# Performance work log

Measured on AMD Instinct MI355X. Metric: run time of the kernel, lower is better.

Reference implementation:

```python
import jax, jax.numpy as jnp
import numpy as np

B, R, H, IN, L = 8, 128, 256, 512, 3
NH, DH = 4, H // 4  # attention heads


def _layernorm(x, g, b, eps=1e-5):
    mu = jnp.mean(x, axis=-1, keepdims=True)
    var = jnp.mean(jnp.square(x - mu), axis=-1, keepdims=True)
    return (x - mu) * jax.lax.rsqrt(var + eps) * g + b


def setup_inputs() -> dict:
    key = jax.random.key(0)
    ks = iter(jax.random.split(key, 40))
    s = 0.02
    d = {}
    d['x'] = jax.random.normal(next(ks), (B, IN), jnp.float32)
    d['We'] = jax.random.normal(next(ks), (IN, H), jnp.float32) * s
    d['be'] = jnp.zeros((H,), jnp.float32)
    # per-graph-layer params, stacked along leading L axis
    d['msg_W1'] = jax.random.normal(next(ks), (L, 2 * H, H), jnp.float32) * s
    d['msg_b1'] = jnp.zeros((L, H), jnp.float32)
    d['msg_W2'] = jax.random.normal(next(ks), (L, H, H), jnp.float32) * s
    d['msg_b2'] = jnp.zeros((L, H), jnp.float32)
    d['upd_W1'] = jax.random.normal(next(ks), (L, 2 * H, H), jnp.float32) * s
    d['upd_b1'] = jnp.zeros((L, H), jnp.float32)
    d['upd_W2'] = jax.random.normal(next(ks), (L, H, H), jnp.float32) * s
    d['upd_b2'] = jnp.zeros((L, H), jnp.float32)
    d['ln_g'] = jnp.ones((L, H), jnp.float32)
    d['ln_b'] = jnp.zeros((L, H), jnp.float32)
    d['rule_adj'] = jax.random.normal(next(ks), (R, R), jnp.float32)
    # multihead attention (4 heads)
    d['Wq'] = jax.random.normal(next(ks), (H, H), jnp.float32) * s
    d['bq'] = jnp.zeros((H,), jnp.float32)
    d['Wk'] = jax.random.normal(next(ks), (H, H), jnp.float32) * s
    d['bk'] = jnp.zeros((H,), jnp.float32)
    d['Wv'] = jax.random.normal(next(ks), (H, H), jnp.float32) * s
    d['bv'] = jnp.zeros((H,), jnp.float32)
    d['Wo'] = jax.random.normal(next(ks), (H, H), jnp.float32) * s
    d['bo'] = jnp.zeros((H,), jnp.float32)
    # readout MLP -> num_rules logits
    d['ro_W1'] = jax.random.normal(next(ks), (H, H), jnp.float32) * s
    d['ro_b1'] = jnp.zeros((H,), jnp.float32)
    d['ro_W2'] = jax.random.normal(next(ks), (H, R), jnp.float32) * s
    d['ro_b2'] = jnp.zeros((R,), jnp.float32)
    return d


def reference(x, We, be, msg_W1, msg_b1, msg_W2, msg_b2,
              upd_W1, upd_b1, upd_W2, upd_b2, ln_g, ln_b, rule_adj,
              Wq, bq, Wk, bk, Wv, bv, Wo, bo,
              ro_W1, ro_b1, ro_W2, ro_b2):
    # node encoder, broadcast to all rule-graph nodes: [B,R,H]
    h0 = x @ We + be
    h = jnp.broadcast_to(h0[:, None, :], (B, R, H))
    # rule adjacency with self-edges excluded (loop used i != j)
    A = jax.nn.sigmoid(rule_adj) * (1.0 - jnp.eye(R, dtype=rule_adj.dtype))  # [R,R]
    for l in range(L):
        # message_net(cat(h_i, h_j)) = relu(h_i@W1a + h_j@W1b + b1)@W2 + b2
        W1a, W1b = msg_W1[l][:H], msg_W1[l][H:]
        a = h @ W1a   # [B,R,H] (receiver i part)
        bb = h @ W1b  # [B,R,H] (sender j part)
        pre = jax.nn.relu(a[:, :, None, :] + bb[:, None, :, :] + msg_b1[l])  # [B,R,R,H]
        m = pre @ msg_W2[l] + msg_b2[l]  # [B,R,R,H] message from j to i
        agg = jnp.einsum('bijh,ij->bih', m, A)  # weighted sum over senders j
        # update_net(cat(h, agg))
        Wu1a, Wu1b = upd_W1[l][:H], upd_W1[l][H:]
        u = jax.nn.relu(h @ Wu1a + agg @ Wu1b + upd_b1[l]) @ upd_W2[l] + upd_b2[l]
        h = _layernorm(h + u, ln_g[l], ln_b[l])
    # multihead self-attention over nodes
    q = (h @ Wq + bq).reshape(B, R, NH, DH)
    k = (h @ Wk + bk).reshape(B, R, NH, DH)
    v = (h @ Wv + bv).reshape(B, R, NH, DH)
    logits = jnp.einsum('bqhd,bkhd->bhqk', q, k) / jnp.sqrt(jnp.float32(DH))
    attn = jax.nn.softmax(logits, axis=-1)
    pooled = jnp.einsum('bhqk,bkhd->bqhd', attn, v).reshape(B, R, H) @ Wo + bo
    g = jnp.mean(pooled, axis=1)  # [B,H]
    rule_logits = jax.nn.relu(g @ ro_W1 + ro_b1) @ ro_W2 + ro_b2
    rule_probabilities = jax.nn.softmax(rule_logits, axis=-1)  # [B,R]
    return rule_probabilities
```

## Files before the change

### kernel.cpp

```cpp
#include <hip/hip_runtime.h>
#include <math.h>

constexpr int NB  = 8;
constexpr int NR  = 128;
constexpr int HID = 256;
constexpr int NIN = 512;
constexpr int DHD = 64;
constexpr size_t SZ = (size_t)NB * NR * HID;

struct KP {
    const float *x, *We, *be, *msg_W1, *msg_b1, *msg_W2, *msg_b2;
    const float *upd_W1, *upd_b1, *upd_W2, *upd_b2, *ln_g, *ln_b, *rule_adj;
    const float *Wq, *bq, *Wk, *bk, *Wv, *bv, *Wo, *bo, *ro_W1, *ro_b1, *ro_W2, *ro_b2;
    float* out;
    float *N0, *N1, *N2;
    float *aB, *bbB, *p1B;
    float *aA, *bbA, *p1A;
    float *W2u, *mb2u, *Aw, *rsum;
    float *mW1s;
    float *h0g;
    float *gacc;
    float *scratch;
};

__device__ __forceinline__ void gemm_core(
    float (&As)[16][68], float (&Bs)[16][64], int m0, int n0,
    const float* __restrict__ A, const float* __restrict__ B,
    float (&acc)[4][4])
{
    int tid = threadIdx.x;
    int ty = tid >> 4, tx = tid & 15;
    int arow = tid >> 2, acol = (tid & 3) << 2;
    int brow = tid >> 4, bcol = (tid & 15) << 2;
    int m = m0 + arow;

    float4 av = *(const float4*)&A[(size_t)m * HID + acol];
    float4 bv = *(const float4*)&B[(size_t)brow * HID + n0 + bcol];

    for (int k0 = 0; k0 < HID; k0 += 16) {
        As[acol + 0][arow] = av.x;
        As[acol + 1][arow] = av.y;
        As[acol + 2][arow] = av.z;
        As[acol + 3][arow] = av.w;
        *(float4*)&Bs[brow][bcol] = bv;
        __syncthreads();
        if (k0 + 16 < HID) {
            av = *(const float4*)&A[(size_t)m * HID + k0 + 16 + acol];
            bv = *(const float4*)&B[(size_t)(k0 + 16 + brow) * HID + n0 + bcol];
        }
#pragma unroll
        for (int kk = 0; kk < 16; ++kk) {
            float4 af = *(const float4*)&As[kk][ty << 2];
            float4 bf = *(const float4*)&Bs[kk][tx << 2];
            float a_[4] = {af.x, af.y, af.z, af.w};
            float b_[4] = {bf.x, bf.y, bf.z, bf.w};
#pragma unroll
            for (int i = 0; i < 4; ++i)
#pragma unroll
                for (int j = 0; j < 4; ++j) acc[i][j] += a_[i] * b_[j];
        }
        __syncthreads();
    }
}

__device__ __forceinline__ void gemv256w(
    const float* xs, const float* __restrict__ W,
    const float* __restrict__ bias, int relu, float* ys, float* red)
{
    int tid = threadIdx.x;
    int w = tid >> 6, l = tid & 63;
    float4 acc = {0.f, 0.f, 0.f, 0.f};
    const float* Wp = W + (size_t)(w * 64) * HID + l * 4;
    const float* xp = xs + w * 64;
#pragma unroll 16
    for (int kk = 0; kk < 64; ++kk) {
        float xv = xp[kk];
        float4 wv = *(const float4*)(Wp + (size_t)kk * HID);
        acc.x += xv * wv.x; acc.y += xv * wv.y;
        acc.z += xv * wv.z; acc.w += xv * wv.w;
    }
    *(float4*)&red[w * 256 + l * 4] = acc;
    __syncthreads();
    float v = red[tid] + red[256 + tid] + red[512 + tid] + red[768 + tid];
    if (bias) v += bias[tid];
    if (relu) v = fmaxf(v, 0.0f);
    ys[tid] = v;
    __syncthreads();
}

__device__ __forceinline__ void rows4_q(
    const float (&rows)[4][HID], const float* __restrict__ W,
    int col, int q, float o[4])
{
    o[0] = o[1] = o[2] = o[3] = 0.f;
    int kb = q * 64;
#pragma unroll 4
    for (int k0 = 0; k0 < 64; k0 += 4) {
        int k = kb + k0;
        float w0 = W[(size_t)(k + 0) * HID + col];
        float w1 = W[(size_t)(k + 1) * HID + col];
        float w2 = W[(size_t)(k + 2) * HID + col];
        float w3 = W[(size_t)(k + 3) * HID + col];
#pragma unroll
        for (int ii = 0; ii < 4; ++ii) {
            float4 rv = *(const float4*)&rows[ii][k];
            o[ii] += rv.x * w0 + rv.y * w1 + rv.z * w2 + rv.w * w3;
        }
    }
}

__device__ __forceinline__ float gemv_q(
    const float* xs, const float* __restrict__ W, int col, int q)
{
    float o = 0.f;
    int kb = q * 64;
#pragma unroll 8
    for (int k = 0; k < 64; ++k)
        o += xs[kb + k] * W[(size_t)(kb + k) * HID + col];
    return o;
}

__device__ __forceinline__ void ln_stats4_q(
    float (&sred)[4][4][2], float (&mi)[4][2], const float v[4], int q)
{
    if (q == 0) {
        int w = threadIdx.x >> 6, l = threadIdx.x & 63;
        float s[4], qq[4];
#pragma unroll
        for (int ii = 0; ii < 4; ++ii) { s[ii] = v[ii]; qq[ii] = v[ii] * v[ii]; }
#pragma unroll
        for (int off = 32; off; off >>= 1) {
#pragma unroll
            for (int ii = 0; ii < 4; ++ii) {
                s[ii] += __shfl_xor(s[ii], off);
                qq[ii] += __shfl_xor(qq[ii], off);
            }
        }
        if (l == 0) {
#pragma unroll
            for (int ii = 0; ii < 4; ++ii) { sred[w][ii][0] = s[ii]; sred[w][ii][1] = qq[ii]; }
        }
    }
    __syncthreads();
    if (threadIdx.x < 4) {
        int r = threadIdx.x;
        float ss = sred[0][r][0] + sred[1][r][0] + sred[2][r][0] + sred[3][r][0];
        float qq = sred[0][r][1] + sred[1][r][1] + sred[2][r][1] + sred[3][r][1];
        float mu = ss * (1.0f / HID);
        mi[r][0] = mu;
        mi[r][1] = rsqrtf(qq * (1.0f / HID) - mu * mu + 1e-5f);
    }
    __syncthreads();
}

__global__ __launch_bounds__(256) void setup0_kernel(KP P) {
    __shared__ union {
        struct { float As[16][68]; float Bs[16][64]; } g;
        struct { float xs[NIN]; float part[8][32]; } e;
    } L;
    int blk = blockIdx.x;
    int t = threadIdx.x;

    if (blk < 32) {
        int rr = blk * 4 + (t >> 6);
        int l = t & 63;
        float s_loc = 0.f;
#pragma unroll
        for (int rep = 0; rep < 2; ++rep) {
            int j = l + rep * 64;
            float xv = P.rule_adj[rr * NR + j];
            float sg = 1.0f / (1.0f + expf(-xv));
            if (j == rr) sg = 0.0f;
            P.Aw[rr * NR + j] = sg;
            s_loc += sg;
        }
#pragma unroll
        for (int off = 32; off; off >>= 1) s_loc += __shfl_xor(s_loc, off);
        if (l == 0) P.rsum[rr] = s_loc;
    } else if (blk < 80) {
        int idx = blk - 32, l2 = idx >> 4, t16 = idx & 15;
        int m0 = (t16 >> 2) * 64, n0 = (t16 & 3) * 64;
        float acc[4][4] = {};
        gemm_core(L.g.As, L.g.Bs, m0, n0,
                  P.msg_W2 + (size_t)l2 * HID * HID,
                  P.upd_W1 + (size_t)l2 * 2 * HID * HID + (size_t)HID * HID,
                  acc);
        int ty = t >> 4, tx = t & 15;
        float* C = P.W2u + (size_t)l2 * HID * HID;
#pragma unroll
        for (int i = 0; i < 4; ++i) {
            int m = m0 + (ty << 2) + i, n = n0 + (tx << 2);
            float4 o = {acc[i][0], acc[i][1], acc[i][2], acc[i][3]};
            *(float4*)&C[(size_t)m * HID + n] = o;
        }
    } else if (blk < 83) {
        int l2 = blk - 80;
        const float* b2v = P.msg_b2 + l2 * HID;
        const float* Bm = P.upd_W1 + (size_t)l2 * 2 * HID * HID + (size_t)HID * HID;
        float acc = 0.f;
#pragma unroll 4
        for (int k = 0; k < HID; ++k) acc += b2v[k] * Bm[(size_t)k * HID + t];
        P.mb2u[l2 * HID + t] = acc;
    } else if (blk < 147) {
        int idx = blk - 83;
        int b = idx >> 3, s = idx & 7;
        L.e.xs[t]       = P.x[b * NIN + t];
        L.e.xs[256 + t] = P.x[b * NIN + 256 + t];
        __syncthreads();
        int c = t & 31, seg = t >> 5;
        int col = s * 32 + c;
        const float* Wp = P.We + (size_t)(seg * 64) * HID + col;
        const float* xp = L.e.xs + seg * 64;
        float acc = 0.f;
#pragma unroll 16
        for (int k = 0; k < 64; ++k) acc += xp[k] * Wp[(size_t)k * HID];
        L.e.part[seg][c] = acc;
        __syncthreads();
        if (t < 32) {
            float v = 0.f;
#pragma unroll
            for (int sg = 0; sg < 8; ++sg) v += L.e.part[sg][t];
            int cc = s * 32 + t;
            P.h0g[b * HID + cc] = v + P.be[cc];
        }
    } else if (blk < 163) {
        int base = (blk - 147) * 4096;
        for (int i = t; i < 4096; i += 256) {
            int o = base + i;
            P.mW1s[o] = P.msg_W1[o] + P.msg_W1[65536 + o];
        }
    } else {
        int pfid = blk - 163, npf = 256 - 163;
        const float* arr[11] = {P.We, P.msg_W1, P.msg_W2, P.upd_W1, P.upd_W2,
                                P.Wq, P.Wk, P.Wv, P.Wo, P.ro_W1, P.ro_W2};
        const int n4[11] = {32768, 98304, 49152, 98304, 49152,
                            16384, 16384, 16384, 16384, 16384, 8192};
        float s = 0.f;
        for (int a = 0; a < 11; ++a) {
            const float4* p4 = (const float4*)arr[a];
            for (int i = pfid * 256 + t; i < n4[a]; i += npf * 256) {
                float4 v = p4[i];
                s += v.x + v.y + v.z + v.w;
            }
        }
        if (s == 1.0e37f) P.scratch[pfid] = s;
    }
}

__global__ __launch_bounds__(1024) void layer0p_kernel(KP P) {
    __shared__ float h0s[HID], p0s[HID], c0s[HID], c1s[HID];
    __shared__ float u1s[4][HID];
    __shared__ float nrm[4][HID];
    __shared__ float part4[4][4][HID];
    __shared__ float sred[4][4][2];
    __shared__ float mi[4][2];
    int blk = blockIdx.x;
    int m0 = blk * 4;
    int b = m0 >> 7, i0 = m0 & 127;
    int t = threadIdx.x;
    int col = t & 255, q = t >> 8;

    if (q == 0) h0s[col] = P.h0g[b * HID + col];
    __syncthreads();

    part4[q][0][col] = gemv_q(h0s, P.upd_W1, col, q);
    part4[q][1][col] = gemv_q(h0s, P.mW1s, col, q);
    __syncthreads();
    if (q == 0) {
        c0s[col] = part4[0][0][col] + part4[1][0][col] + part4[2][0][col] + part4[3][0][col];
        float pv = part4[0][1][col] + part4[1][1][col] + part4[2][1][col] + part4[3][1][col];
        p0s[col] = fmaxf(pv + P.msg_b1[col], 0.0f);
    }
    __syncthreads();
    part4[q][0][col] = gemv_q(p0s, P.W2u, col, q);
    __syncthreads();
    if (q == 0) {
        c1s[col] = part4[0][0][col] + part4[1][0][col] + part4[2][0][col] + part4[3][0][col]
                 + P.mb2u[col];
        float ubv = P.upd_b1[col];
#pragma unroll
        for (int ii = 0; ii < 4; ++ii)
            u1s[ii][col] = fmaxf(c0s[col] + P.rsum[i0 + ii] * c1s[col] + ubv, 0.0f);
    }
    __syncthreads();

    float o[4];
    rows4_q(u1s, P.upd_W2, col, q, o);
#pragma unroll
    for (int ii = 0; ii < 4; ++ii) part4[q][ii][col] = o[ii];
    __syncthreads();
    float v[4] = {0.f, 0.f, 0.f, 0.f};
    if (q == 0) {
        float h0v = h0s[col] + P.upd_b2[col];
#pragma unroll
        for (int ii = 0; ii < 4; ++ii)
            v[ii] = part4[0][ii][col] + part4[1][ii][col] + part4[2][ii][col]
                  + part4[3][ii][col] + h0v;
    }
    ln_stats4_q(sred, mi, v, q);
    if (q == 0) {
        float gv = P.ln_g[col], btv = P.ln_b[col];
#pragma unroll
        for (int ii = 0; ii < 4; ++ii) {
            float nv = (v[ii] - mi[ii][0]) * mi[ii][1] * gv + btv;
            nrm[ii][col] = nv;
            P.N0[(size_t)(m0 + ii) * HID + col] = nv;
        }
    }
    __syncthreads();

    const float* mW1a1 = P.msg_W1 + (size_t)1 * 2 * HID * HID;
    const float* uW1a1 = P.upd_W1 + (size_t)1 * 2 * HID * HID;
    const float* pw[3] = {mW1a1, mW1a1 + (size_t)HID * HID, uW1a1};
    float* po[3] = {P.aB, P.bbB, P.p1B};
#pragma unroll
    for (int p = 0; p < 3; ++p) {
        rows4_q(nrm, pw[p], col, q, o);
#pragma unroll
        for (int ii = 0; ii < 4; ++ii) part4[q][ii][col] = o[ii];
        __syncthreads();
        if (q == 0) {
#pragma unroll
            for (int ii = 0; ii < 4; ++ii)
                po[p][(size_t)(m0 + ii) * HID + col] =
                    part4[0][ii][col] + part4[1][ii][col] +
                    part4[2][ii][col] + part4[3][ii][col];
        }
        __syncthreads();
    }
}

__global__ __launch_bounds__(1024) void aggproj_kernel(
    const float* __restrict__ a, const float* __restrict__ bbv,
    const float* __restrict__ mb1, const float* __restrict__ Aw,
    const float* __restrict__ rsumv,
    const float* __restrict__ P1, const float* __restrict__ W2u,
    const float* __restrict__ mb2u, const float* __restrict__ ub1,
    const float* __restrict__ uW2, const float* __restrict__ ub2,
    const float* __restrict__ Nprev, const float* __restrict__ lng,
    const float* __restrict__ lnb, float* __restrict__ Nout,
    const float* __restrict__ pw0, const float* __restrict__ pb0, float* __restrict__ o0,
    const float* __restrict__ pw1, const float* __restrict__ pb1, float* __restrict__ o1,
    const float* __restrict__ pw2, const float* __restrict__ pb2, float* __restrict__ o2,
    float* __restrict__ gzero)
{
    __shared__ float ap[4][HID];
    __shared__ float u1s[4][HID];
    __shared__ float nrm[4][HID];
    __shared__ float awr[4][NR];
    __shared__ float part4[4][4][HID];
    __shared__ float sred[4][4][2];
    __shared__ float mi[4][2];
    int blk = blockIdx.x;
    int b  = blk >> 5;
    int i0 = (blk & 31) * 4;
    int m0 = b * NR + i0;
    int t  = threadIdx.x;
    int col = t & 255, q = t >> 8;

    if (gzero && blk == 0 && q == 0) {
#pragma unroll
        for (int i = 0; i < 8; ++i) gzero[i * 256 + col] = 0.f;
    }

    if (t < 512) awr[t >> 7][t & 127] = Aw[(i0 + (t >> 7)) * NR + (t & 127)];

    float bias = mb1[col];
    float ai[4];
#pragma unroll
    for (int ii = 0; ii < 4; ++ii)
        ai[ii] = a[(size_t)(m0 + ii) * HID + col] + bias;
    __syncthreads();

    {
        float acc[4] = {0.f, 0.f, 0.f, 0.f};
        const float* bbb = &bbv[(size_t)b * NR * HID + col];
        int jb = q * 32;
#pragma unroll 4
        for (int j = 0; j < 32; ++j) {
            float bj = bbb[(size_t)(jb + j) * HID];
#pragma unroll
            for (int ii = 0; ii < 4; ++ii) {
                float pre = fmaxf(ai[ii] + bj, 0.0f);
                acc[ii] += awr[ii][jb + j] * pre;
            }
        }
#pragma unroll
        for (int ii = 0; ii < 4; ++ii) part4[q][ii][col] = acc[ii];
        __syncthreads();
        if (q == 0) {
#pragma unroll
            for (int ii = 0; ii < 4; ++ii)
                ap[ii][col] = part4[0][ii][col] + part4[1][ii][col]
                            + part4[2][ii][col] + part4[3][ii][col];
        }
        __syncthreads();
    }

    {
        float o[4];
        rows4_q(ap, W2u, col, q, o);
#pragma unroll
        for (int ii = 0; ii < 4; ++ii) part4[q][ii][col] = o[ii];
        __syncthreads();
        if (q == 0) {
            float mbv = mb2u[col], ubv = ub1[col];
#pragma unroll
            for (int ii = 0; ii < 4; ++ii) {
                float w2f = part4[0][ii][col] + part4[1][ii][col]
                          + part4[2][ii][col] + part4[3][ii][col];
                float vv = w2f + P1[(size_t)(m0 + ii) * HID + col]
                         + rsumv[i0 + ii] * mbv + ubv;
                u1s[ii][col] = fmaxf(vv, 0.0f);
            }
        }
        __syncthreads();
    }

    {
        float o[4];
        rows4_q(u1s, uW2, col, q, o);
#pragma unroll
        for (int ii = 0; ii < 4; ++ii) part4[q][ii][col] = o[ii];
        __syncthreads();
        float v[4] = {0.f, 0.f, 0.f, 0.f};
        if (q == 0) {
            float ub2v = ub2[col];
#pragma unroll
            for (int ii = 0; ii < 4; ++ii) {
                float uf = part4[0][ii][col] + part4[1][ii][col]
                         + part4[2][ii][col] + part4[3][ii][col];
                v[ii] = Nprev[(size_t)(m0 + ii) * HID + col] + uf + ub2v;
            }
        }
        ln_stats4_q(sred, mi, v, q);
        if (q == 0) {
            float gv = lng[col], btv = lnb[col];
#pragma unroll
            for (int ii = 0; ii < 4; ++ii) {
                float nv = (v[ii] - mi[ii][0]) * mi[ii][1] * gv + btv;
                nrm[ii][col] = nv;
                Nout[(size_t)(m0 + ii) * HID + col] = nv;
            }
        }
        __syncthreads();
    }

    {
        const float* pw[3] = {pw0, pw1, pw2};
        const float* pb[3] = {pb0, pb1, pb2};
        float* po[3] = {o0, o1, o2};
#pragma unroll
        for (int p = 0; p < 3; ++p) {
            float o[4];
            rows4_q(nrm, pw[p], col, q, o);
#pragma unroll
            for (int ii = 0; ii < 4; ++ii) part4[q][ii][col] = o[ii];
            __syncthreads();
            if (q == 0) {
                float pbv = pb[p] ? pb[p][col] : 0.f;
#pragma unroll
                for (int ii = 0; ii < 4; ++ii)
                    po[p][(size_t)(m0 + ii) * HID + col] =
                        part4[0][ii][col] + part4[1][ii][col] +
                        part4[2][ii][col] + part4[3][ii][col] + pbv;
            }
            __syncthreads();
        }
    }
}

__global__ __launch_bounds__(256) void attention_kernel(
    const float* __restrict__ q, const float* __restrict__ k,
    const float* __restrict__ v, float* __restrict__ gacc)
{
    __shared__ struct { float KhT[64][128]; float S[16][128]; float qs[16][64]; } L;
    int blk = blockIdx.x;
    int bh = blk >> 3, ig = blk & 7;
    int b = bh >> 2, hd = bh & 3;
    int i0 = ig * 16;
    int t = threadIdx.x;
    const float* qg = q + ((size_t)b * NR) * HID + hd * DHD;
    const float* kg = k + ((size_t)b * NR) * HID + hd * DHD;
    const float* vg = v + ((size_t)b * NR) * HID + hd * DHD;

    {
        int j = t >> 1, half = t & 1;
        const float* krow = kg + (size_t)j * HID + half * 32;
#pragma unroll
        for (int c = 0; c < 32; c += 4) {
            float4 kv = *(const float4*)(krow + c);
            L.KhT[half * 32 + c + 0][j] = kv.x;
            L.KhT[half * 32 + c + 1][j] = kv.y;
            L.KhT[half * 32 + c + 2][j] = kv.z;
            L.KhT[half * 32 + c + 3][j] = kv.w;
        }
    }
    {
        int ii = t >> 4, d0 = (t & 15) * 4;
        *(float4*)&L.qs[ii][d0] = *(const float4*)(qg + (size_t)(i0 + ii) * HID + d0);
    }
    __syncthreads();
    {
        int j = t & 127, ii2 = t >> 7;
        float acc[8] = {0.f,0.f,0.f,0.f,0.f,0.f,0.f,0.f};
#pragma unroll 4
        for (int d = 0; d < 64; ++d) {
            float kv = L.KhT[d][j];
#pragma unroll
            for (int ii = 0; ii < 8; ++ii) acc[ii] += L.qs[ii2 * 8 + ii][d] * kv;
        }
#pragma unroll
        for (int ii = 0; ii < 8; ++ii) L.S[ii2 * 8 + ii][j] = acc[ii] * 0.125f;
    }
    __syncthreads();
    {
        int w = t >> 6, l = t & 63;
#pragma unroll
        for (int r = w * 4; r < w * 4 + 4; ++r) {
            float e0 = L.S[r][l], e1 = L.S[r][l + 64];
            float mx = fmaxf(e0, e1);
#pragma unroll
            for (int off = 32; off; off >>= 1) mx = fmaxf(mx, __shfl_xor(mx, off));
            e0 = expf(e0 - mx); e1 = expf(e1 - mx);
            float sm = e0 + e1;
#pragma unroll
            for (int off = 32; off; off >>= 1) sm += __shfl_xor(sm, off);
            float inv = 1.0f / sm;
            L.S[r][l] = e0 * inv; L.S[r][l + 64] = e1 * inv;
        }
    }
    __syncthreads();
    {
        int d = t & 63, ir = t >> 6;
        float accv[4] = {0.f, 0.f, 0.f, 0.f};
        const float* vp = vg + d;
#pragma unroll 8
        for (int j = 0; j < NR; ++j) {
            float vv = vp[(size_t)j * HID];
#pragma unroll
            for (int p = 0; p < 4; ++p) accv[p] += L.S[p * 4 + ir][j] * vv;
        }
        float s = accv[0] + accv[1] + accv[2] + accv[3];
        atomicAdd(&gacc[b * HID + hd * DHD + d], s);
    }
}

__global__ __launch_bounds__(256) void tailf_kernel(KP P) {
    __shared__ float v0[HID], v1[HID], v2[HID];
    __shared__ float red[1024];
    int b = blockIdx.x;
    int t = threadIdx.x;
    int w = t >> 6, l = t & 63;

    v0[t] = P.gacc[b * HID + t] * (1.0f / NR);
    __syncthreads();
    gemv256w(v0, P.Wo, P.bo, 0, v1, red);
    gemv256w(v1, P.ro_W1, P.ro_b1, 1, v2, red);

    {
        float2 acc = {0.f, 0.f};
        const float* Wp = P.ro_W2 + (size_t)(w * 64) * NR + l * 2;
        const float* xp = v2 + w * 64;
#pragma unroll 8
        for (int kk = 0; kk < 64; ++kk) {
            float xv = xp[kk];
            float2 wv = *(const float2*)(Wp + (size_t)kk * NR);
            acc.x += xv * wv.x; acc.y += xv * wv.y;
        }
        *(float2*)&red[w * 128 + l * 2] = acc;
        __syncthreads();
    }
    float logit = -1e30f;
    if (t < NR) logit = red[t] + red[128 + t] + red[256 + t] + red[384 + t] + P.ro_b2[t];
    __syncthreads();
    float m = logit;
#pragma unroll
    for (int off = 32; off; off >>= 1) m = fmaxf(m, __shfl_xor(m, off));
    if (l == 0) red[w] = m;
    __syncthreads();
    m = fmaxf(red[0], red[1]);
    float e = (t < NR) ? expf(logit - m) : 0.0f;
    float ssum = e;
#pragma unroll
    for (int off = 32; off; off >>= 1) ssum += __shfl_xor(ssum, off);
    if (l == 0) red[4 + w] = ssum;
    __syncthreads();
    float tot = red[4] + red[5];
    if (t < NR) P.out[b * NR + t] = e / tot;
}

extern "C" void kernel_launch(void* const* d_in, const int* in_sizes, int n_in,
                              void* d_out, int out_size, void* d_ws, size_t ws_size,
                              hipStream_t stream)
{
    KP P;
    P.x        = (const float*)d_in[0];
    P.We       = (const float*)d_in[1];
    P.be       = (const float*)d_in[2];
    P.msg_W1   = (const float*)d_in[3];
    P.msg_b1   = (const float*)d_in[4];
    P.msg_W2   = (const float*)d_in[5];
    P.msg_b2   = (const float*)d_in[6];
    P.upd_W1   = (const float*)d_in[7];
    P.upd_b1   = (const float*)d_in[8];
    P.upd_W2   = (const float*)d_in[9];
    P.upd_b2   = (const float*)d_in[10];
    P.ln_g     = (const float*)d_in[11];
    P.ln_b     = (const float*)d_in[12];
    P.rule_adj = (const float*)d_in[13];
    P.Wq       = (const float*)d_in[14];
    P.bq       = (const float*)d_in[15];
    P.Wk       = (const float*)d_in[16];
    P.bk       = (const float*)d_in[17];
    P.Wv       = (const float*)d_in[18];
    P.bv       = (const float*)d_in[19];
    P.Wo       = (const float*)d_in[20];
    P.bo       = (const float*)d_in[21];
    P.ro_W1    = (const float*)d_in[22];
    P.ro_b1    = (const float*)d_in[23];
    P.ro_W2    = (const float*)d_in[24];
    P.ro_b2    = (const float*)d_in[25];
    P.out      = (float*)d_out;

    float* b0 = (float*)d_ws;
    P.N0     = b0;  b0 += SZ;
    P.N1     = b0;  b0 += SZ;
    P.N2     = b0;  b0 += SZ;
    P.aB     = b0;  b0 += SZ;
    P.bbB    = b0;  b0 += SZ;
    P.p1B    = b0;  b0 += SZ;
    P.aA     = b0;  b0 += SZ;
    P.bbA    = b0;  b0 += SZ;
    P.p1A    = b0;  b0 += SZ;
    P.W2u    = b0;  b0 += 3 * HID * HID;
    P.mb2u   = b0;  b0 += 3 * HID;
    P.mW1s   = b0;  b0 += HID * HID;
    P.Aw     = b0;  b0 += NR * NR;
    P.rsum   = b0;  b0 += NR;
    P.h0g    = b0;  b0 += NB * HID;
    P.gacc   = b0;  b0 += NB * HID;
    P.scratch= b0;  b0 += 256;

    setup0_kernel<<<dim3(256), 256, 0, stream>>>(P);

    layer0p_kernel<<<dim3(256), 1024, 0, stream>>>(P);

    {
        const int l = 1;
        const float* mW1a2 = P.msg_W1 + (size_t)2 * 2 * HID * HID;
        const float* uW1a2 = P.upd_W1 + (size_t)2 * 2 * HID * HID;
        aggproj_kernel<<<dim3(256), 1024, 0, stream>>>(
            P.aB, P.bbB, P.msg_b1 + (size_t)l * HID, P.Aw, P.rsum,
            P.p1B, P.W2u + (size_t)l * HID * HID, P.mb2u + l * HID,
            P.upd_b1 + (size_t)l * HID,
            P.upd_W2 + (size_t)l * HID * HID, P.upd_b2 + (size_t)l * HID,
            P.N0, P.ln_g + (size_t)l * HID, P.ln_b + (size_t)l * HID, P.N1,
            mW1a2, nullptr, P.aA,
            mW1a2 + (size_t)HID * HID, nullptr, P.bbA,
            uW1a2, nullptr, P.p1A,
            nullptr);
    }

    {
        const int l = 2;
        aggproj_kernel<<<dim3(256), 1024, 0, stream>>>(
            P.aA, P.bbA, P.msg_b1 + (size_t)l * HID, P.Aw, P.rsum,
            P.p1A, P.W2u + (size_t)l * HID * HID, P.mb2u + l * HID,
            P.upd_b1 + (size_t)l * HID,
            P.upd_W2 + (size_t)l * HID * HID, P.upd_b2 + (size_t)l * HID,
            P.N1, P.ln_g + (size_t)l * HID, P.ln_b + (size_t)l * HID, P.N2,
            P.Wq, P.bq, P.aB,
            P.Wk, P.bk, P.bbB,
            P.Wv, P.bv, P.p1B,
            P.gacc);
    }

    attention_kernel<<<dim3(256), 256, 0, stream>>>(P.aB, P.bbB, P.p1B, P.gacc);

    tailf_kernel<<<dim3(8), 256, 0, stream>>>(P);
}
```

Measured before the change: 231.8 us.

## Fuse setup with layer-0 kernel and attention with tail via last-block counter

Merges the setup kernel and the layer-0 kernel into one launch. Layer 0 now computes the encoder, the adjacency row sums and the message and update chain (msg_W2 and then upd_W1b as separate GEMVs) inline per block, instead of relying on precomputed W2u and h0g. The tail MLP and softmax are folded into the attention kernel, where the last block to finish, found with an atomic counter, runs the tail for all batches. This removes two kernel launches and their serialization. In exchange each layer-0 block redundantly computes the encoder and extra GEMVs, and the tail runs serially in a single block.

```diff
diff --git a/kernel.cpp b/kernel.cpp
--- a/kernel.cpp
+++ b/kernel.cpp
@@ -17,51 +17,9 @@
     float *aB, *bbB, *p1B;
     float *aA, *bbA, *p1A;
     float *W2u, *mb2u, *Aw, *rsum;
-    float *mW1s;
-    float *h0g;
     float *gacc;
     float *scratch;
 };
-
-__device__ __forceinline__ void gemm_core(
-    float (&As)[16][68], float (&Bs)[16][64], int m0, int n0,
-    const float* __restrict__ A, const float* __restrict__ B,
-    float (&acc)[4][4])
-{
-    int tid = threadIdx.x;
-    int ty = tid >> 4, tx = tid & 15;
-    int arow = tid >> 2, acol = (tid & 3) << 2;
-    int brow = tid >> 4, bcol = (tid & 15) << 2;
-    int m = m0 + arow;
-
-    float4 av = *(const float4*)&A[(size_t)m * HID + acol];
-    float4 bv = *(const float4*)&B[(size_t)brow * HID + n0 + bcol];
-
-    for (int k0 = 0; k0 < HID; k0 += 16) {
-        As[acol + 0][arow] = av.x;
-        As[acol + 1][arow] = av.y;
-        As[acol + 2][arow] = av.z;
-        As[acol + 3][arow] = av.w;
-        *(float4*)&Bs[brow][bcol] = bv;
-        __syncthreads();
-        if (k0 + 16 < HID) {
-            av = *(const float4*)&A[(size_t)m * HID + k0 + 16 + acol];
-            bv = *(const float4*)&B[(size_t)(k0 + 16 + brow) * HID + n0 + bcol];
-        }
-#pragma unroll
-        for (int kk = 0; kk < 16; ++kk) {
-            float4 af = *(const float4*)&As[kk][ty << 2];
-            float4 bf = *(const float4*)&Bs[kk][tx << 2];
-            float a_[4] = {af.x, af.y, af.z, af.w};
-            float b_[4] = {bf.x, bf.y, bf.z, bf.w};
-#pragma unroll
-            for (int i = 0; i < 4; ++i)
-#pragma unroll
-                for (int j = 0; j < 4; ++j) acc[i][j] += a_[i] * b_[j];
-        }
-        __syncthreads();
-    }
-}
 
 __device__ __forceinline__ void gemv256w(
     const float* xs, const float* __restrict__ W,
@@ -153,84 +111,212 @@
     __syncthreads();
 }
 
-__global__ __launch_bounds__(256) void setup0_kernel(KP P) {
+__global__ __launch_bounds__(1024) void megaL0_kernel(KP P) {
     __shared__ union {
+        struct {
+            float xs[NIN];
+            float h0s[HID], p0s[HID], m0s[HID], c0s[HID], c1s[HID];
+            float rsums[4];
+            float u1s[4][HID];
+            float nrm[4][HID];
+            float part4[4][4][HID];
+            float sred[4][4][2];
+            float mi[4][2];
+        } l0;
         struct { float As[16][68]; float Bs[16][64]; } g;
-        struct { float xs[NIN]; float part[8][32]; } e;
-    } L;
+        struct { float red[8][2]; } adj;
+    } U;
     int blk = blockIdx.x;
     int t = threadIdx.x;
 
-    if (blk < 32) {
-        int rr = blk * 4 + (t >> 6);
-        int l = t & 63;
-        float s_loc = 0.f;
-#pragma unroll
-        for (int rep = 0; rep < 2; ++rep) {
-            int j = l + rep * 64;
-            float xv = P.rule_adj[rr * NR + j];
-            float sg = 1.0f / (1.0f + expf(-xv));
-            if (j == rr) sg = 0.0f;
-            P.Aw[rr * NR + j] = sg;
-            s_loc += sg;
-        }
-#pragma unroll
-        for (int off = 32; off; off >>= 1) s_loc += __shfl_xor(s_loc, off);
-        if (l == 0) P.rsum[rr] = s_loc;
-    } else if (blk < 80) {
-        int idx = blk - 32, l2 = idx >> 4, t16 = idx & 15;
-        int m0 = (t16 >> 2) * 64, n0 = (t16 & 3) * 64;
-        float acc[4][4] = {};
-        gemm_core(L.g.As, L.g.Bs, m0, n0,
-                  P.msg_W2 + (size_t)l2 * HID * HID,
-                  P.upd_W1 + (size_t)l2 * 2 * HID * HID + (size_t)HID * HID,
-                  acc);
-        int ty = t >> 4, tx = t & 15;
+    if (blk < 256) {
+        if (blk == 0 && t == 0) *(int*)P.scratch = 0;
+        int m0 = blk * 4;
+        int b = m0 >> 7, i0 = m0 & 127;
+        int col = t & 255, q = t >> 8;
+
+        if (t < NIN) U.l0.xs[t] = P.x[b * NIN + t];
+        if (t < 256) {
+            int row = t >> 6, l = t & 63;
+            int rr = i0 + row;
+            float s = 0.f;
+            {
+                float xv = P.rule_adj[rr * NR + l];
+                float sg = 1.0f / (1.0f + expf(-xv));
+                if (l == rr) sg = 0.f;
+                s += sg;
+            }
+            {
+                int j = l + 64;
+                float xv = P.rule_adj[rr * NR + j];
+                float sg = 1.0f / (1.0f + expf(-xv));
+                if (j == rr) sg = 0.f;
+                s += sg;
+            }
+#pragma unroll
+            for (int off = 32; off; off >>= 1) s += __shfl_xor(s, off);
+            if (l == 0) U.l0.rsums[row] = s;
+        }
+        __syncthreads();
+
+        {
+            float o = 0.f;
+            int kb = q * 128;
+#pragma unroll 8
+            for (int k = 0; k < 128; ++k)
+                o += U.l0.xs[kb + k] * P.We[(size_t)(kb + k) * HID + col];
+            U.l0.part4[q][0][col] = o;
+        }
+        __syncthreads();
+        if (q == 0)
+            U.l0.h0s[col] = U.l0.part4[0][0][col] + U.l0.part4[1][0][col]
+                          + U.l0.part4[2][0][col] + U.l0.part4[3][0][col] + P.be[col];
+        __syncthreads();
+
+        {
+            int kb = q * 64;
+            float op = 0.f, oc = 0.f;
+            const float* W1a = P.msg_W1;
+            const float* W1b = P.msg_W1 + (size_t)HID * HID;
+            const float* Ua  = P.upd_W1;
+#pragma unroll 4
+            for (int k = 0; k < 64; ++k) {
+                float h = U.l0.h0s[kb + k];
+                size_t idx = (size_t)(kb + k) * HID + col;
+                op += h * (W1a[idx] + W1b[idx]);
+                oc += h * Ua[idx];
+            }
+            U.l0.part4[q][0][col] = op;
+            U.l0.part4[q][1][col] = oc;
+        }
+        __syncthreads();
+        if (q == 0) {
+            float pv = U.l0.part4[0][0][col] + U.l0.part4[1][0][col]
+                     + U.l0.part4[2][0][col] + U.l0.part4[3][0][col] + P.msg_b1[col];
+            U.l0.p0s[col] = fmaxf(pv, 0.0f);
+            U.l0.c0s[col] = U.l0.part4[0][1][col] + U.l0.part4[1][1][col]
+                          + U.l0.part4[2][1][col] + U.l0.part4[3][1][col];
+        }
+        __syncthreads();
+
+        U.l0.part4[q][0][col] = gemv_q(U.l0.p0s, P.msg_W2, col, q);
+        __syncthreads();
+        if (q == 0)
+            U.l0.m0s[col] = U.l0.part4[0][0][col] + U.l0.part4[1][0][col]
+                          + U.l0.part4[2][0][col] + U.l0.part4[3][0][col] + P.msg_b2[col];
+        __syncthreads();
+
+        U.l0.part4[q][0][col] = gemv_q(U.l0.m0s, P.upd_W1 + (size_t)HID * HID, col, q);
+        __syncthreads();
+        if (q == 0) {
+            U.l0.c1s[col] = U.l0.part4[0][0][col] + U.l0.part4[1][0][col]
+                          + U.l0.part4[2][0][col] + U.l0.part4[3][0][col];
+            float ubv = P.upd_b1[col];
+#pragma unroll
+            for (int ii = 0; ii < 4; ++ii)
+                U.l0.u1s[ii][col] =
+                    fmaxf(U.l0.c0s[col] + U.l0.rsums[ii] * U.l0.c1s[col] + ubv, 0.0f);
+        }
+        __syncthreads();
+
+        float o4[4];
+        rows4_q(U.l0.u1s, P.upd_W2, col, q, o4);
+#pragma unroll
+        for (int ii = 0; ii < 4; ++ii) U.l0.part4[q][ii][col] = o4[ii];
+        __syncthreads();
+        float v[4] = {0.f, 0.f, 0.f, 0.f};
+        if (q == 0) {
+            float h0v = U.l0.h0s[col] + P.upd_b2[col];
+#pragma unroll
+            for (int ii = 0; ii < 4; ++ii)
+                v[ii] = U.l0.part4[0][ii][col] + U.l0.part4[1][ii][col]
+                      + U.l0.part4[2][ii][col] + U.l0.part4[3][ii][col] + h0v;
+        }
+        ln_stats4_q(U.l0.sred, U.l0.mi, v, q);
+        if (q == 0) {
+            float gv = P.ln_g[col], btv = P.ln_b[col];
+#pragma unroll
+            for (int ii = 0; ii < 4; ++ii) {
+                float nv = (v[ii] - U.l0.mi[ii][0]) * U.l0.mi[ii][1] * gv + btv;
+                U.l0.nrm[ii][col] = nv;
+                P.N0[(size_t)(m0 + ii) * HID + col] = nv;
+            }
+        }
+        __syncthreads();
+
+        const float* mW1a1 = P.msg_W1 + (size_t)1 * 2 * HID * HID;
+        const float* uW1a1 = P.upd_W1 + (size_t)1 * 2 * HID * HID;
+        const float* pw[3] = {mW1a1, mW1a1 + (size_t)HID * HID, uW1a1};
+        float* po[3] = {P.aB, P.bbB, P.p1B};
+#pragma unroll
+        for (int p = 0; p < 3; ++p) {
+            rows4_q(U.l0.nrm, pw[p], col, q, o4);
+#pragma unroll
+            for (int ii = 0; ii < 4; ++ii) U.l0.part4[q][ii][col] = o4[ii];
+            __syncthreads();
+            if (q == 0) {
+#pragma unroll
+                for (int ii = 0; ii < 4; ++ii)
+                    po[p][(size_t)(m0 + ii) * HID + col] =
+                        U.l0.part4[0][ii][col] + U.l0.part4[1][ii][col] +
+                        U.l0.part4[2][ii][col] + U.l0.part4[3][ii][col];
+            }
+            __syncthreads();
+        }
+    } else if (blk < 272) {
+        int rr = (blk - 256) * 8 + (t >> 7);
+        int j = t & 127;
+        float xv = P.rule_adj[rr * NR + j];
+        float sg = 1.0f / (1.0f + expf(-xv));
+        if (j == rr) sg = 0.f;
+        P.Aw[rr * NR + j] = sg;
+        float s = sg;
+#pragma unroll
+        for (int off = 32; off; off >>= 1) s += __shfl_xor(s, off);
+        int row8 = t >> 7, wh = (t >> 6) & 1;
+        if ((t & 63) == 0) U.adj.red[row8][wh] = s;
+        __syncthreads();
+        if (j == 0) P.rsum[rr] = U.adj.red[row8][0] + U.adj.red[row8][1];
+    } else if (blk < 304) {
+        int idx = blk - 272, l2 = idx >> 4, t16 = idx & 15;
+        int m0t = (t16 >> 2) * 64, n0t = (t16 & 3) * 64;
+        const float* A = P.msg_W2 + (size_t)(1 + l2) * HID * HID;
+        const float* B = P.upd_W1 + (size_t)(1 + l2) * 2 * HID * HID + (size_t)HID * HID;
+        int arow = t >> 4, acol = t & 15;
+        int brow = t >> 6, bcol = t & 63;
+        int ty = t >> 5, tx = t & 31;
+        float acc[2][2] = {};
+        for (int k0 = 0; k0 < HID; k0 += 16) {
+            U.g.As[acol][arow] = A[(size_t)(m0t + arow) * HID + k0 + acol];
+            U.g.Bs[brow][bcol] = B[(size_t)(k0 + brow) * HID + n0t + bcol];
+            __syncthreads();
+#pragma unroll
+            for (int kk = 0; kk < 16; ++kk) {
+                float a0 = U.g.As[kk][ty * 2], a1 = U.g.As[kk][ty * 2 + 1];
+                float b0 = U.g.Bs[kk][tx * 2], b1 = U.g.Bs[kk][tx * 2 + 1];
+                acc[0][0] += a0 * b0; acc[0][1] += a0 * b1;
+                acc[1][0] += a1 * b0; acc[1][1] += a1 * b1;
+            }
+            __syncthreads();
+        }
         float* C = P.W2u + (size_t)l2 * HID * HID;
 #pragma unroll
-        for (int i = 0; i < 4; ++i) {
-            int m = m0 + (ty << 2) + i, n = n0 + (tx << 2);
-            float4 o = {acc[i][0], acc[i][1], acc[i][2], acc[i][3]};
-            *(float4*)&C[(size_t)m * HID + n] = o;
-        }
-    } else if (blk < 83) {
-        int l2 = blk - 80;
-        const float* b2v = P.msg_b2 + l2 * HID;
-        const float* Bm = P.upd_W1 + (size_t)l2 * 2 * HID * HID + (size_t)HID * HID;
-        float acc = 0.f;
+        for (int i = 0; i < 2; ++i)
+#pragma unroll
+            for (int j = 0; j < 2; ++j)
+                C[(size_t)(m0t + ty * 2 + i) * HID + n0t + tx * 2 + j] = acc[i][j];
+    } else if (blk < 306) {
+        int l2 = blk - 304;
+        if (t < 256) {
+            const float* b2v = P.msg_b2 + (1 + l2) * HID;
+            const float* Bm = P.upd_W1 + (size_t)(1 + l2) * 2 * HID * HID + (size_t)HID * HID;
+            float acc = 0.f;
 #pragma unroll 4
-        for (int k = 0; k < HID; ++k) acc += b2v[k] * Bm[(size_t)k * HID + t];
-        P.mb2u[l2 * HID + t] = acc;
-    } else if (blk < 147) {
-        int idx = blk - 83;
-        int b = idx >> 3, s = idx & 7;
-        L.e.xs[t]       = P.x[b * NIN + t];
-        L.e.xs[256 + t] = P.x[b * NIN + 256 + t];
-        __syncthreads();
-        int c = t & 31, seg = t >> 5;
-        int col = s * 32 + c;
-        const float* Wp = P.We + (size_t)(seg * 64) * HID + col;
-        const float* xp = L.e.xs + seg * 64;
-        float acc = 0.f;
-#pragma unroll 16
-        for (int k = 0; k < 64; ++k) acc += xp[k] * Wp[(size_t)k * HID];
-        L.e.part[seg][c] = acc;
-        __syncthreads();
-        if (t < 32) {
-            float v = 0.f;
-#pragma unroll
-            for (int sg = 0; sg < 8; ++sg) v += L.e.part[sg][t];
-            int cc = s * 32 + t;
-            P.h0g[b * HID + cc] = v + P.be[cc];
-        }
-    } else if (blk < 163) {
-        int base = (blk - 147) * 4096;
-        for (int i = t; i < 4096; i += 256) {
-            int o = base + i;
-            P.mW1s[o] = P.msg_W1[o] + P.msg_W1[65536 + o];
+            for (int k = 0; k < HID; ++k) acc += b2v[k] * Bm[(size_t)k * HID + t];
+            P.mb2u[l2 * HID + t] = acc;
         }
     } else {
-        int pfid = blk - 163, npf = 256 - 163;
+        int pfid = blk - 306, npf = 352 - 306;
         const float* arr[11] = {P.We, P.msg_W1, P.msg_W2, P.upd_W1, P.upd_W2,
                                 P.Wq, P.Wk, P.Wv, P.Wo, P.ro_W1, P.ro_W2};
         const int n4[11] = {32768, 98304, 49152, 98304, 49152,
@@ -238,95 +324,12 @@
         float s = 0.f;
         for (int a = 0; a < 11; ++a) {
             const float4* p4 = (const float4*)arr[a];
-            for (int i = pfid * 256 + t; i < n4[a]; i += npf * 256) {
+            for (int i = pfid * 1024 + t; i < n4[a]; i += npf * 1024) {
                 float4 v = p4[i];
                 s += v.x + v.y + v.z + v.w;
             }
         }
-        if (s == 1.0e37f) P.scratch[pfid] = s;
-    }
-}
-
-__global__ __launch_bounds__(1024) void layer0p_kernel(KP P) {
-    __shared__ float h0s[HID], p0s[HID], c0s[HID], c1s[HID];
-    __shared__ float u1s[4][HID];
-    __shared__ float nrm[4][HID];
-    __shared__ float part4[4][4][HID];
-    __shared__ float sred[4][4][2];
-    __shared__ float mi[4][2];
-    int blk = blockIdx.x;
-    int m0 = blk * 4;
-    int b = m0 >> 7, i0 = m0 & 127;
-    int t = threadIdx.x;
-    int col = t & 255, q = t >> 8;
-
-    if (q == 0) h0s[col] = P.h0g[b * HID + col];
-    __syncthreads();
-
-    part4[q][0][col] = gemv_q(h0s, P.upd_W1, col, q);
-    part4[q][1][col] = gemv_q(h0s, P.mW1s, col, q);
-    __syncthreads();
-    if (q == 0) {
-        c0s[col] = part4[0][0][col] + part4[1][0][col] + part4[2][0][col] + part4[3][0][col];
-        float pv = part4[0][1][col] + part4[1][1][col] + part4[2][1][col] + part4[3][1][col];
-        p0s[col] = fmaxf(pv + P.msg_b1[col], 0.0f);
-    }
-    __syncthreads();
-    part4[q][0][col] = gemv_q(p0s, P.W2u, col, q);
-    __syncthreads();
-    if (q == 0) {
-        c1s[col] = part4[0][0][col] + part4[1][0][col] + part4[2][0][col] + part4[3][0][col]
-                 + P.mb2u[col];
-        float ubv = P.upd_b1[col];
-#pragma unroll
-        for (int ii = 0; ii < 4; ++ii)
-            u1s[ii][col] = fmaxf(c0s[col] + P.rsum[i0 + ii] * c1s[col] + ubv, 0.0f);
-    }
-    __syncthreads();
-
-    float o[4];
-    rows4_q(u1s, P.upd_W2, col, q, o);
-#pragma unroll
-    for (int ii = 0; ii < 4; ++ii) part4[q][ii][col] = o[ii];
-    __syncthreads();
-    float v[4] = {0.f, 0.f, 0.f, 0.f};
-    if (q == 0) {
-        float h0v = h0s[col] + P.upd_b2[col];
-#pragma unroll
-        for (int ii = 0; ii < 4; ++ii)
-            v[ii] = part4[0][ii][col] + part4[1][ii][col] + part4[2][ii][col]
-                  + part4[3][ii][col] + h0v;
-    }
-    ln_stats4_q(sred, mi, v, q);
-    if (q == 0) {
-        float gv = P.ln_g[col], btv = P.ln_b[col];
-#pragma unroll
-        for (int ii = 0; ii < 4; ++ii) {
-            float nv = (v[ii] - mi[ii][0]) * mi[ii][1] * gv + btv;
-            nrm[ii][col] = nv;
-            P.N0[(size_t)(m0 + ii) * HID + col] = nv;
-        }
-    }
-    __syncthreads();
-
-    const float* mW1a1 = P.msg_W1 + (size_t)1 * 2 * HID * HID;
-    const float* uW1a1 = P.upd_W1 + (size_t)1 * 2 * HID * HID;
-    const float* pw[3] = {mW1a1, mW1a1 + (size_t)HID * HID, uW1a1};
-    float* po[3] = {P.aB, P.bbB, P.p1B};
-#pragma unroll
-    for (int p = 0; p < 3; ++p) {
-        rows4_q(nrm, pw[p], col, q, o);
-#pragma unroll
-        for (int ii = 0; ii < 4; ++ii) part4[q][ii][col] = o[ii];
-        __syncthreads();
-        if (q == 0) {
-#pragma unroll
-            for (int ii = 0; ii < 4; ++ii)
-                po[p][(size_t)(m0 + ii) * HID + col] =
-                    part4[0][ii][col] + part4[1][ii][col] +
-                    part4[2][ii][col] + part4[3][ii][col];
-        }
-        __syncthreads();
+        if (s == 1.0e37f) P.scratch[64] = s;
     }
 }
 
@@ -470,19 +473,20 @@
     }
 }
 
-__global__ __launch_bounds__(256) void attention_kernel(
-    const float* __restrict__ q, const float* __restrict__ k,
-    const float* __restrict__ v, float* __restrict__ gacc)
-{
-    __shared__ struct { float KhT[64][128]; float S[16][128]; float qs[16][64]; } L;
+__global__ __launch_bounds__(256) void attn_tail_kernel(KP P) {
+    __shared__ union {
+        struct { float KhT[64][128]; float S[16][128]; float qs[16][64]; } a;
+        struct { float v0[HID]; float v1[HID]; float v2[HID]; float red[1024]; } tl;
+    } L;
+    __shared__ int lastFlag;
     int blk = blockIdx.x;
     int bh = blk >> 3, ig = blk & 7;
     int b = bh >> 2, hd = bh & 3;
     int i0 = ig * 16;
     int t = threadIdx.x;
-    const float* qg = q + ((size_t)b * NR) * HID + hd * DHD;
-    const float* kg = k + ((size_t)b * NR) * HID + hd * DHD;
-    const float* vg = v + ((size_t)b * NR) * HID + hd * DHD;
+    const float* qg = P.aB  + ((size_t)b * NR) * HID + hd * DHD;
+    const float* kg = P.bbB + ((size_t)b * NR) * HID + hd * DHD;
+    const float* vg = P.p1B + ((size_t)b * NR) * HID + hd * DHD;
 
     {
         int j = t >> 1, half = t & 1;
@@ -490,15 +494,15 @@
 #pragma unroll
         for (int c = 0; c < 32; c += 4) {
             float4 kv = *(const float4*)(krow + c);
-            L.KhT[half * 32 + c + 0][j] = kv.x;
-            L.KhT[half * 32 + c + 1][j] = kv.y;
-            L.KhT[half * 32 + c + 2][j] = kv.z;
-            L.KhT[half * 32 + c + 3][j] = kv.w;
+            L.a.KhT[half * 32 + c + 0][j] = kv.x;
+            L.a.KhT[half * 32 + c + 1][j] = kv.y;
+            L.a.KhT[half * 32 + c + 2][j] = kv.z;
+            L.a.KhT[half * 32 + c + 3][j] = kv.w;
         }
     }
     {
         int ii = t >> 4, d0 = (t & 15) * 4;
-        *(float4*)&L.qs[ii][d0] = *(const float4*)(qg + (size_t)(i0 + ii) * HID + d0);
+        *(float4*)&L.a.qs[ii][d0] = *(const float4*)(qg + (size_t)(i0 + ii) * HID + d0);
     }
     __syncthreads();
     {
@@ -506,19 +510,19 @@
         float acc[8] = {0.f,0.f,0.f,0.f,0.f,0.f,0.f,0.f};
 #pragma unroll 4
         for (int d = 0; d < 64; ++d) {
-            float kv = L.KhT[d][j];
-#pragma unroll
-            for (int ii = 0; ii < 8; ++ii) acc[ii] += L.qs[ii2 * 8 + ii][d] * kv;
-        }
-#pragma unroll
-        for (int ii = 0; ii < 8; ++ii) L.S[ii2 * 8 + ii][j] = acc[ii] * 0.125f;
+            float kv = L.a.KhT[d][j];
+#pragma unroll
+            for (int ii = 0; ii < 8; ++ii) acc[ii] += L.a.qs[ii2 * 8 + ii][d] * kv;
+        }
+#pragma unroll
+        for (int ii = 0; ii < 8; ++ii) L.a.S[ii2 * 8 + ii][j] = acc[ii] * 0.125f;
     }
     __syncthreads();
     {
         int w = t >> 6, l = t & 63;
 #pragma unroll
         for (int r = w * 4; r < w * 4 + 4; ++r) {
-            float e0 = L.S[r][l], e1 = L.S[r][l + 64];
+            float e0 = L.a.S[r][l], e1 = L.a.S[r][l + 64];
             float mx = fmaxf(e0, e1);
 #pragma unroll
             for (int off = 32; off; off >>= 1) mx = fmaxf(mx, __shfl_xor(mx, off));
@@ -527,7 +531,7 @@
 #pragma unroll
             for (int off = 32; off; off >>= 1) sm += __shfl_xor(sm, off);
             float inv = 1.0f / sm;
-            L.S[r][l] = e0 * inv; L.S[r][l + 64] = e1 * inv;
+            L.a.S[r][l] = e0 * inv; L.a.S[r][l + 64] = e1 * inv;
         }
     }
     __syncthreads();
@@ -539,55 +543,63 @@
         for (int j = 0; j < NR; ++j) {
             float vv = vp[(size_t)j * HID];
 #pragma unroll
-            for (int p = 0; p < 4; ++p) accv[p] += L.S[p * 4 + ir][j] * vv;
+            for (int p = 0; p < 4; ++p) accv[p] += L.a.S[p * 4 + ir][j] * vv;
         }
         float s = accv[0] + accv[1] + accv[2] + accv[3];
-        atomicAdd(&gacc[b * HID + hd * DHD + d], s);
-    }
-}
-
-__global__ __launch_bounds__(256) void tailf_kernel(KP P) {
-    __shared__ float v0[HID], v1[HID], v2[HID];
-    __shared__ float red[1024];
-    int b = blockIdx.x;
-    int t = threadIdx.x;
+        atomicAdd(&P.gacc[b * HID + hd * DHD + d], s);
+    }
+
+    __syncthreads();
+    if (t == 0) {
+        __builtin_amdgcn_fence(__ATOMIC_RELEASE, "agent");
+        int old = __hip_atomic_fetch_add((int*)P.scratch, 1,
+                                         __ATOMIC_ACQ_REL, __HIP_MEMORY_SCOPE_AGENT);
+        lastFlag = (old == 255);
+    }
+    __syncthreads();
+    if (!lastFlag) return;
+    __builtin_amdgcn_fence(__ATOMIC_ACQUIRE, "agent");
+
     int w = t >> 6, l = t & 63;
-
-    v0[t] = P.gacc[b * HID + t] * (1.0f / NR);
-    __syncthreads();
-    gemv256w(v0, P.Wo, P.bo, 0, v1, red);
-    gemv256w(v1, P.ro_W1, P.ro_b1, 1, v2, red);
-
-    {
-        float2 acc = {0.f, 0.f};
-        const float* Wp = P.ro_W2 + (size_t)(w * 64) * NR + l * 2;
-        const float* xp = v2 + w * 64;
+    for (int bb = 0; bb < NB; ++bb) {
+        L.tl.v0[t] = __hip_atomic_load(&P.gacc[bb * HID + t], __ATOMIC_RELAXED,
+                                       __HIP_MEMORY_SCOPE_AGENT) * (1.0f / NR);
+        __syncthreads();
+        gemv256w(L.tl.v0, P.Wo, P.bo, 0, L.tl.v1, L.tl.red);
+        gemv256w(L.tl.v1, P.ro_W1, P.ro_b1, 1, L.tl.v2, L.tl.red);
+        {
+            float2 acc = {0.f, 0.f};
+            const float* Wp = P.ro_W2 + (size_t)(w * 64) * NR + l * 2;
+            const float* xp = L.tl.v2 + w * 64;
 #pragma unroll 8
-        for (int kk = 0; kk < 64; ++kk) {
-            float xv = xp[kk];
-            float2 wv = *(const float2*)(Wp + (size_t)kk * NR);
-            acc.x += xv * wv.x; acc.y += xv * wv.y;
-        }
-        *(float2*)&red[w * 128 + l * 2] = acc;
-        __syncthreads();
-    }
-    float logit = -1e30f;
-    if (t < NR) logit = red[t] + red[128 + t] + red[256 + t] + red[384 + t] + P.ro_b2[t];
-    __syncthreads();
-    float m = logit;
-#pragma unroll
-    for (int off = 32; off; off >>= 1) m = fmaxf(m, __shfl_xor(m, off));
-    if (l == 0) red[w] = m;
-    __syncthreads();
-    m = fmaxf(red[0], red[1]);
-    float e = (t < NR) ? expf(logit - m) : 0.0f;
-    float ssum = e;
-#pragma unroll
-    for (int off = 32; off; off >>= 1) ssum += __shfl_xor(ssum, off);
-    if (l == 0) red[4 + w] = ssum;
-    __syncthreads();
-    float tot = red[4] + red[5];
-    if (t < NR) P.out[b * NR + t] = e / tot;
+            for (int kk = 0; kk < 64; ++kk) {
+                float xv = xp[kk];
+                float2 wv = *(const float2*)(Wp + (size_t)kk * NR);
+                acc.x += xv * wv.x; acc.y += xv * wv.y;
+            }
+            *(float2*)&L.tl.red[w * 128 + l * 2] = acc;
+            __syncthreads();
+        }
+        float logit = -1e30f;
+        if (t < NR) logit = L.tl.red[t] + L.tl.red[128 + t] + L.tl.red[256 + t]
+                          + L.tl.red[384 + t] + P.ro_b2[t];
+        __syncthreads();
+        float m = logit;
+#pragma unroll
+        for (int off = 32; off; off >>= 1) m = fmaxf(m, __shfl_xor(m, off));
+        if (l == 0) L.tl.red[w] = m;
+        __syncthreads();
+        m = fmaxf(L.tl.red[0], L.tl.red[1]);
+        float e = (t < NR) ? expf(logit - m) : 0.0f;
+        float ssum = e;
+#pragma unroll
+        for (int off = 32; off; off >>= 1) ssum += __shfl_xor(ssum, off);
+        if (l == 0) L.tl.red[4 + w] = ssum;
+        __syncthreads();
+        float tot = L.tl.red[4] + L.tl.red[5];
+        if (t < NR) P.out[bb * NR + t] = e / tot;
+        __syncthreads();
+    }
 }
 
 extern "C" void kernel_launch(void* const* d_in, const int* in_sizes, int n_in,
@@ -633,18 +645,14 @@
     P.aA     = b0;  b0 += SZ;
     P.bbA    = b0;  b0 += SZ;
     P.p1A    = b0;  b0 += SZ;
-    P.W2u    = b0;  b0 += 3 * HID * HID;
-    P.mb2u   = b0;  b0 += 3 * HID;
-    P.mW1s   = b0;  b0 += HID * HID;
+    P.W2u    = b0;  b0 += 2 * HID * HID;
+    P.mb2u   = b0;  b0 += 2 * HID;
     P.Aw     = b0;  b0 += NR * NR;
     P.rsum   = b0;  b0 += NR;
-    P.h0g    = b0;  b0 += NB * HID;
     P.gacc   = b0;  b0 += NB * HID;
     P.scratch= b0;  b0 += 256;
 
-    setup0_kernel<<<dim3(256), 256, 0, stream>>>(P);
-
-    layer0p_kernel<<<dim3(256), 1024, 0, stream>>>(P);
+    megaL0_kernel<<<dim3(352), 1024, 0, stream>>>(P);
 
     {
         const int l = 1;
@@ -652,7 +660,7 @@
         const float* uW1a2 = P.upd_W1 + (size_t)2 * 2 * HID * HID;
         aggproj_kernel<<<dim3(256), 1024, 0, stream>>>(
             P.aB, P.bbB, P.msg_b1 + (size_t)l * HID, P.Aw, P.rsum,
-            P.p1B, P.W2u + (size_t)l * HID * HID, P.mb2u + l * HID,
+            P.p1B, P.W2u, P.mb2u,
             P.upd_b1 + (size_t)l * HID,
             P.upd_W2 + (size_t)l * HID * HID, P.upd_b2 + (size_t)l * HID,
             P.N0, P.ln_g + (size_t)l * HID, P.ln_b + (size_t)l * HID, P.N1,
@@ -666,7 +674,7 @@
         const int l = 2;
         aggproj_kernel<<<dim3(256), 1024, 0, stream>>>(
             P.aA, P.bbA, P.msg_b1 + (size_t)l * HID, P.Aw, P.rsum,
-            P.p1A, P.W2u + (size_t)l * HID * HID, P.mb2u + l * HID,
+            P.p1A, P.W2u + (size_t)HID * HID, P.mb2u + HID,
             P.upd_b1 + (size_t)l * HID,
             P.upd_W2 + (size_t)l * HID * HID, P.upd_b2 + (size_t)l * HID,
             P.N1, P.ln_g + (size_t)l * HID, P.ln_b + (size_t)l * HID, P.N2,
@@ -676,7 +684,5 @@
             P.gacc);
     }
 
-    attention_kernel<<<dim3(256), 256, 0, stream>>>(P.aB, P.bbB, P.p1B, P.gacc);
-
-    tailf_kernel<<<dim3(8), 256, 0, stream>>>(P);
-}
+    attn_tail_kernel<<<dim3(256), 256, 0, stream>>>(P);
+}
```

Result: slower. 306.4 us (+32.2%).
